# Optimization experiments

Measured on AMD Instinct MI355X. Metric: run time of the kernel, lower is better.

The kernel has to match this reference:

```python
import jax, jax.numpy as jnp
import numpy as np

N_NODES = 50000
N_EDGES = 800000
N_FEAT = 512
N_HID = 256
N_LAYER = 4
N_CLASS = 40


def setup_inputs() -> dict:
    key = jax.random.key(0)
    ks = jax.random.split(key, 16)
    x = jax.random.normal(ks[0], (N_NODES, N_FEAT), dtype=jnp.float32)
    edge_index = jax.random.randint(ks[1], (2, N_EDGES), 0, N_NODES, dtype=jnp.int64 if jax.config.jax_enable_x64 else jnp.int32)

    def glorot(k, fan_in, fan_out):
        lim = np.sqrt(6.0 / (fan_in + fan_out)).astype(np.float32)
        return jax.random.uniform(k, (fan_in, fan_out), jnp.float32, -lim, lim)

    in_gc_W = glorot(ks[2], N_FEAT, N_HID)
    in_gc_b = jnp.zeros((N_HID,), jnp.float32)
    in_lin_W = glorot(ks[3], N_FEAT, N_HID)
    in_lin_b = jnp.zeros((N_HID,), jnp.float32)
    # n_layer-1 = 3 hidden conv / lin pairs, stacked on leading axis
    convs_W = jnp.stack([glorot(jax.random.fold_in(ks[4], i), N_HID, N_HID) for i in range(N_LAYER - 1)])
    convs_b = jnp.zeros((N_LAYER - 1, N_HID), jnp.float32)
    lins_W = jnp.stack([glorot(jax.random.fold_in(ks[5], i), N_HID, N_HID) for i in range(N_LAYER - 1)])
    lins_b = jnp.zeros((N_LAYER - 1, N_HID), jnp.float32)
    out_W = glorot(ks[6], N_HID * N_LAYER, N_CLASS)
    out_b = jnp.zeros((N_CLASS,), jnp.float32)
    return {
        "x": x, "edge_index": edge_index,
        "in_gc_W": in_gc_W, "in_gc_b": in_gc_b,
        "in_lin_W": in_lin_W, "in_lin_b": in_lin_b,
        "convs_W": convs_W, "convs_b": convs_b,
        "lins_W": lins_W, "lins_b": lins_b,
        "out_W": out_W, "out_b": out_b,
    }


def reference(x, edge_index, in_gc_W, in_gc_b, in_lin_W, in_lin_b,
              convs_W, convs_b, lins_W, lins_b, out_W, out_b):
    src, dst = edge_index[0], edge_index[1]
    n = x.shape[0]
    # GCN symmetric normalization with self-loops: deg = 1 + in-degree
    deg = jnp.zeros((n,), jnp.float32).at[dst].add(1.0) + 1.0
    dinv = jax.lax.rsqrt(deg)
    edge_norm = dinv[src] * dinv[dst]        # [E]
    self_norm = dinv * dinv                  # [N]

    def gcn(h, W, b):
        hw = h @ W                           # [N, out]
        msg = hw[src] * edge_norm[:, None]   # gather + scale
        agg = jax.ops.segment_sum(msg, dst, num_segments=n)
        agg = agg + hw * self_norm[:, None]  # self-loop term
        return agg + b

    # inductive: GCNConv + linear residual; dropout = identity (eval mode)
    h = jax.nn.relu(gcn(x, in_gc_W, in_gc_b) + x @ in_lin_W + in_lin_b)
    xs = [h]
    for i in range(convs_W.shape[0]):
        h = jax.nn.relu(gcn(h, convs_W[i], convs_b[i]) + h @ lins_W[i] + lins_b[i])
        xs.append(h)
    # JumpingKnowledge mode='cat'
    jk = jnp.concatenate(xs, axis=-1)        # [N, n_hid * n_layer]
    return jk @ out_W + out_b
```

## Files before the change

### kernel.cpp

```cpp
#include <hip/hip_runtime.h>

typedef _Float16 half8 __attribute__((ext_vector_type(8)));
typedef _Float16 half4 __attribute__((ext_vector_type(4)));
typedef float floatx4 __attribute__((ext_vector_type(4)));

__device__ __forceinline__ void gld16(const _Float16* g, _Float16* lds_base) {
    __builtin_amdgcn_global_load_lds(
        (const __attribute__((address_space(1))) unsigned int*)g,
        (__attribute__((address_space(3))) unsigned int*)lds_base,
        16, 0, 0);
}

__global__ __launch_bounds__(256) void zero_i32(int* __restrict__ p, int n) {
    int i = blockIdx.x * 256 + threadIdx.x;
    if (i < n) p[i] = 0;
}

__global__ __launch_bounds__(256) void hist_dst(const int* __restrict__ dst,
                                                int* __restrict__ count, int E) {
    int e = blockIdx.x * 256 + threadIdx.x;
    if (e < E) atomicAdd(&count[dst[e]], 1);
}

__global__ __launch_bounds__(256) void make_dinv(const int* __restrict__ count,
                                                 float* __restrict__ dinv, int n) {
    int i = blockIdx.x * 256 + threadIdx.x;
    if (i < n) dinv[i] = rsqrtf(1.0f + (float)count[i]);
}

__global__ __launch_bounds__(256) void cast_f32_f16(const float* __restrict__ in,
                                                    _Float16* __restrict__ out, int n4) {
    int i = blockIdx.x * 256 + threadIdx.x;
    if (i < n4) {
        float4 v = *(const float4*)&in[(size_t)i * 4];
        half4 h = { (_Float16)v.x, (_Float16)v.y, (_Float16)v.z, (_Float16)v.w };
        *(half4*)&out[(size_t)i * 4] = h;
    }
}

__global__ __launch_bounds__(256) void transpose_cast(const float* __restrict__ W,
                                                      _Float16* __restrict__ WT,
                                                      int K, int N) {
    int k = blockIdx.x;
    int n = threadIdx.x;
    if (n < N) WT[(size_t)n * K + k] = (_Float16)W[(size_t)k * N + n];
}

__global__ __launch_bounds__(256) void scan_block(const int* __restrict__ count,
                                                  int* __restrict__ incl,
                                                  int* __restrict__ blocksum, int n) {
    __shared__ int tmp[256];
    int t = threadIdx.x;
    int i = blockIdx.x * 256 + t;
    int v = (i < n) ? count[i] : 0;
    tmp[t] = v;
    __syncthreads();
    for (int off = 1; off < 256; off <<= 1) {
        int x = (t >= off) ? tmp[t - off] : 0;
        __syncthreads();
        tmp[t] += x;
        __syncthreads();
    }
    if (i < n) incl[i] = tmp[t];
    if (t == 255) blocksum[blockIdx.x] = tmp[255];
}

__global__ __launch_bounds__(256) void scan_top(const int* __restrict__ blocksum,
                                                int* __restrict__ blockoff, int nb) {
    __shared__ int tmp[256];
    int t = threadIdx.x;
    int v = (t < nb) ? blocksum[t] : 0;
    tmp[t] = v;
    __syncthreads();
    for (int off = 1; off < 256; off <<= 1) {
        int x = (t >= off) ? tmp[t - off] : 0;
        __syncthreads();
        tmp[t] += x;
        __syncthreads();
    }
    if (t < nb) blockoff[t] = tmp[t] - v;
}

__global__ __launch_bounds__(256) void make_rowptr(const int* __restrict__ incl,
                                                   const int* __restrict__ count,
                                                   const int* __restrict__ blockoff,
                                                   int* __restrict__ rowptr,
                                                   int* __restrict__ cursor, int n) {
    int i = blockIdx.x * 256 + threadIdx.x;
    if (i < n) {
        int r = incl[i] - count[i] + blockoff[blockIdx.x];
        rowptr[i] = r;
        cursor[i] = r;
    }
}

__global__ __launch_bounds__(256) void scatter_perm(const int* __restrict__ src,
                                                    const int* __restrict__ dst,
                                                    const float* __restrict__ dinv,
                                                    int* __restrict__ cursor,
                                                    int* __restrict__ sorted_src,
                                                    float* __restrict__ sorted_norm, int E) {
    int e = blockIdx.x * 256 + threadIdx.x;
    if (e < E) {
        int d = dst[e], s = src[e];
        int slot = atomicAdd(&cursor[d], 1);
        sorted_src[slot] = s;
        sorted_norm[slot] = dinv[s] * dinv[d];
    }
}

template<bool DUAL>
__global__ __launch_bounds__(256) void gemm_mfma(
    const _Float16* __restrict__ A, int lda,
    const _Float16* __restrict__ BT, int Nrows,
    const float* __restrict__ bias0, const float* __restrict__ bias1,
    _Float16* __restrict__ lin_h, _Float16* __restrict__ hw,
    float* __restrict__ Cf, int ldc,
    int M, int K)
{
    __shared__ _Float16 As[128 * 64];
    __shared__ _Float16 Bs[128 * 64];

    const int tid  = threadIdx.x;
    const int wave = tid >> 6;
    const int lane = tid & 63;
    const int q    = lane >> 4;
    const int r    = lane & 15;

    const int wm = (wave & 1) * 64;
    const int wn = (wave >> 1) * 64;

    const int bn = blockIdx.x * 128;
    const int bm = blockIdx.y * 128;

    const int srow  = wave * 32;
    const int lrow8 = lane >> 3;
    const int cp    = lane & 7;

    floatx4 acc[4][4] = {};

    for (int k0 = 0; k0 < K; k0 += 64) {
        #pragma unroll
        for (int t = 0; t < 4; ++t) {
            int lrow = srow + t * 8 + lrow8;
            int c    = cp ^ (lrow & 7);
            int gm = bm + lrow; if (gm > M - 1) gm = M - 1;
            gld16(&A[(size_t)gm * lda + k0 + c * 8], &As[(srow + t * 8) * 64]);
            int gn = bn + lrow; if (gn > Nrows - 1) gn = Nrows - 1;
            gld16(&BT[(size_t)gn * K + k0 + c * 8], &Bs[(srow + t * 8) * 64]);
        }
        __syncthreads();

        #pragma unroll
        for (int kk = 0; kk < 2; ++kk) {
            const int sc = ((kk << 2) | q) ^ (r & 7);
            half8 af[4], bf[4];
            #pragma unroll
            for (int mi = 0; mi < 4; ++mi)
                af[mi] = *(const half8*)&As[(wm + mi * 16 + r) * 64 + sc * 8];
            #pragma unroll
            for (int ni = 0; ni < 4; ++ni)
                bf[ni] = *(const half8*)&Bs[(wn + ni * 16 + r) * 64 + sc * 8];
            #pragma unroll
            for (int mi = 0; mi < 4; ++mi)
                #pragma unroll
                for (int ni = 0; ni < 4; ++ni)
                    acc[mi][ni] = __builtin_amdgcn_mfma_f32_16x16x32_f16(
                        af[mi], bf[ni], acc[mi][ni], 0, 0, 0);
        }
        __syncthreads();
    }

    if (DUAL) {
        const bool islin = (bn < 256);
        _Float16* dstp = islin ? lin_h : hw;
        #pragma unroll
        for (int ni = 0; ni < 4; ++ni) {
            int col = bn + wn + ni * 16 + r;
            int c2  = islin ? col : col - 256;
            float badd = islin ? (bias0[col] + bias1[col]) : 0.0f;
            #pragma unroll
            for (int mi = 0; mi < 4; ++mi)
                #pragma unroll
                for (int reg = 0; reg < 4; ++reg) {
                    int gm = bm + wm + mi * 16 + q * 4 + reg;
                    if (gm < M)
                        dstp[(size_t)gm * 256 + c2] = (_Float16)(acc[mi][ni][reg] + badd);
                }
        }
    } else {
        #pragma unroll
        for (int ni = 0; ni < 4; ++ni) {
            int col = bn + wn + ni * 16 + r;
            if (col >= Nrows) continue;
            float badd = bias0 ? bias0[col] : 0.0f;
            #pragma unroll
            for (int mi = 0; mi < 4; ++mi)
                #pragma unroll
                for (int reg = 0; reg < 4; ++reg) {
                    int gm = bm + wm + mi * 16 + q * 4 + reg;
                    if (gm < M)
                        Cf[(size_t)gm * ldc + col] = acc[mi][ni][reg] + badd;
                }
        }
    }
}

__global__ __launch_bounds__(256) void aggregate_csr(
    const int* __restrict__ rowptr, const int* __restrict__ count,
    const int* __restrict__ sorted_src, const float* __restrict__ sorted_norm,
    const float* __restrict__ dinv,
    const _Float16* __restrict__ hw,
    const _Float16* __restrict__ lin_h,
    _Float16* __restrict__ jk_col, int n)
{
    int wave = (blockIdx.x * 256 + threadIdx.x) >> 6;
    int lane = threadIdx.x & 63;
    if (wave >= n) return;
    const int i = wave;

    const int start = rowptr[i];
    const int deg   = count[i];

    half4 l4 = *(const half4*)&lin_h[(size_t)i * 256 + lane * 4];
    float4 acc = make_float4((float)l4[0], (float)l4[1], (float)l4[2], (float)l4[3]);

    for (int base = 0; base < deg; base += 64) {
        int m = deg - base;
        if (m > 64) m = 64;
        int   s_l  = 0;
        float nm_l = 0.0f;
        if (lane < m) {
            s_l  = sorted_src[start + base + lane];
            nm_l = sorted_norm[start + base + lane];
        }
        for (int j = 0; j < m; j += 4) {
            half4 hv[4];
            float nm[4];
            #pragma unroll
            for (int k2 = 0; k2 < 4; ++k2) {
                int jj  = j + k2;
                int idx = (jj < m) ? jj : (m - 1);
                int s   = __shfl(s_l, idx, 64);
                nm[k2]  = (jj < m) ? __shfl(nm_l, jj, 64) : 0.0f;
                hv[k2]  = *(const half4*)&hw[(size_t)s * 256 + lane * 4];
            }
            #pragma unroll
            for (int k2 = 0; k2 < 4; ++k2) {
                acc.x = fmaf((float)hv[k2][0], nm[k2], acc.x);
                acc.y = fmaf((float)hv[k2][1], nm[k2], acc.y);
                acc.z = fmaf((float)hv[k2][2], nm[k2], acc.z);
                acc.w = fmaf((float)hv[k2][3], nm[k2], acc.w);
            }
        }
    }

    float di = dinv[i];
    float sn = di * di;
    half4 hs = *(const half4*)&hw[(size_t)i * 256 + lane * 4];
    acc.x = fmaxf(fmaf((float)hs[0], sn, acc.x), 0.0f);
    acc.y = fmaxf(fmaf((float)hs[1], sn, acc.y), 0.0f);
    acc.z = fmaxf(fmaf((float)hs[2], sn, acc.z), 0.0f);
    acc.w = fmaxf(fmaf((float)hs[3], sn, acc.w), 0.0f);

    half4 o = { (_Float16)acc.x, (_Float16)acc.y, (_Float16)acc.z, (_Float16)acc.w };
    *(half4*)&jk_col[(size_t)i * 1024 + lane * 4] = o;
}

extern "C" void kernel_launch(void* const* d_in, const int* in_sizes, int n_in,
                              void* d_out, int out_size, void* d_ws, size_t ws_size,
                              hipStream_t stream) {
    const float* x        = (const float*)d_in[0];
    const int*   ei       = (const int*)d_in[1];
    const float* in_gc_W  = (const float*)d_in[2];
    const float* in_gc_b  = (const float*)d_in[3];
    const float* in_lin_W = (const float*)d_in[4];
    const float* in_lin_b = (const float*)d_in[5];
    const float* convs_W  = (const float*)d_in[6];
    const float* convs_b  = (const float*)d_in[7];
    const float* lins_W   = (const float*)d_in[8];
    const float* lins_b   = (const float*)d_in[9];
    const float* out_W    = (const float*)d_in[10];
    const float* out_b    = (const float*)d_in[11];

    const int N = 50000;
    const int E = in_sizes[1] / 2;
    const int F = 512, H = 256, L = 4, NC = 40;

    const int* src = ei;
    const int* dst = ei + E;

    char* ws = (char*)d_ws;
    auto carve = [&](size_t bytes) { void* p = ws; ws += (bytes + 255) & ~(size_t)255; return p; };
    float*    dinv       = (float*)carve((size_t)N * 4);
    int*      count      = (int*)  carve((size_t)N * 4);
    int*      incl       = (int*)  carve((size_t)N * 4);
    int*      rowptr     = (int*)  carve((size_t)N * 4);
    int*      cursor     = (int*)  carve((size_t)N * 4);
    int*      blocksum   = (int*)  carve(256 * 4);
    int*      blockoff   = (int*)  carve(256 * 4);
    int*      sorted_src = (int*)  carve((size_t)E * 4);
    float*    sorted_nrm = (float*)carve((size_t)E * 4);
    _Float16* xh         = (_Float16*)carve((size_t)N * F * 2);
    _Float16* w0comb     = (_Float16*)carve((size_t)512 * F * 2);
    _Float16* wcomb      = (_Float16*)carve((size_t)3 * 512 * H * 2);
    _Float16* outWT      = (_Float16*)carve((size_t)NC * H * L * 2);
    _Float16* lin_h      = (_Float16*)carve((size_t)N * H * 2);
    _Float16* hw         = (_Float16*)carve((size_t)N * H * 2);
    _Float16* jk_h       = (_Float16*)carve((size_t)N * H * L * 2);
    float*    out        = (float*)d_out;

    const int nbN = (N + 255) / 256;
    const int nbE = (E + 255) / 256;

    zero_i32<<<nbN, 256, 0, stream>>>(count, N);
    hist_dst<<<nbE, 256, 0, stream>>>(dst, count, E);
    make_dinv<<<nbN, 256, 0, stream>>>(count, dinv, N);
    scan_block<<<nbN, 256, 0, stream>>>(count, incl, blocksum, N);
    scan_top<<<1, 256, 0, stream>>>(blocksum, blockoff, nbN);
    make_rowptr<<<nbN, 256, 0, stream>>>(incl, count, blockoff, rowptr, cursor, N);
    scatter_perm<<<nbE, 256, 0, stream>>>(src, dst, dinv, cursor, sorted_src, sorted_nrm, E);

    cast_f32_f16<<<(N * F / 4 + 255) / 256, 256, 0, stream>>>(x, xh, N * F / 4);
    transpose_cast<<<F, 256, 0, stream>>>(in_lin_W, w0comb,               F, H);
    transpose_cast<<<F, 256, 0, stream>>>(in_gc_W,  w0comb + (size_t)H * F, F, H);
    for (int l = 0; l < 3; ++l) {
        _Float16* wl = wcomb + (size_t)l * 512 * H;
        transpose_cast<<<H, 256, 0, stream>>>(lins_W  + (size_t)l * H * H, wl,                   H, H);
        transpose_cast<<<H, 256, 0, stream>>>(convs_W + (size_t)l * H * H, wl + (size_t)H * H,   H, H);
    }
    transpose_cast<<<H * L, 256, 0, stream>>>(out_W, outWT, H * L, NC);

    const dim3 dgrid(4, (N + 127) / 128);
    const dim3 ogrid(1, (N + 127) / 128);
    const int agg_blocks = (N + 3) / 4;

    for (int l = 0; l < L; ++l) {
        const _Float16* Ah = (l == 0) ? xh : (jk_h + (size_t)(l - 1) * H);
        int lda            = (l == 0) ? F : H * L;
        int K              = (l == 0) ? F : H;
        const _Float16* BT = (l == 0) ? w0comb : (wcomb + (size_t)(l - 1) * 512 * H);
        const float* gcB   = (l == 0) ? in_gc_b  : (convs_b + (size_t)(l - 1) * H);
        const float* liB   = (l == 0) ? in_lin_b : (lins_b  + (size_t)(l - 1) * H);

        gemm_mfma<true><<<dgrid, 256, 0, stream>>>(Ah, lda, BT, 512, liB, gcB,
                                                   lin_h, hw, nullptr, 0, N, K);
        aggregate_csr<<<agg_blocks, 256, 0, stream>>>(rowptr, count, sorted_src, sorted_nrm,
                                                      dinv, hw, lin_h, jk_h + (size_t)l * H, N);
    }

    gemm_mfma<false><<<ogrid, 256, 0, stream>>>(jk_h, H * L, outWT, NC, out_b, nullptr,
                                                nullptr, nullptr, out, NC, N, H * L);
}
```

Before: 746.5 us.

## Pack CSR metadata, widen aggregation loads, fuse dinv, tile weight transposes

Stores each edge's source index and normalisation together as an int2, so aggregation does one load and two shuffles per edge instead of two separate arrays. The aggregation kernel now splits each wave into two half-waves that each read 16-byte half8 rows for alternating edges, then combines the halves with an xor-shuffle. That doubles the edges in flight per iteration but performs a cross-lane reduction and leaves half the lanes idle at the store. Separately, dinv is computed inside scan_block, removing one launch, and the weight transposes use a 32x32 LDS-tiled kernel for coalesced writes.

```diff
diff --git a/kernel.cpp b/kernel.cpp
--- a/kernel.cpp
+++ b/kernel.cpp
@@ -20,12 +20,6 @@
                                                 int* __restrict__ count, int E) {
     int e = blockIdx.x * 256 + threadIdx.x;
     if (e < E) atomicAdd(&count[dst[e]], 1);
-}
-
-__global__ __launch_bounds__(256) void make_dinv(const int* __restrict__ count,
-                                                 float* __restrict__ dinv, int n) {
-    int i = blockIdx.x * 256 + threadIdx.x;
-    if (i < n) dinv[i] = rsqrtf(1.0f + (float)count[i]);
 }
 
 __global__ __launch_bounds__(256) void cast_f32_f16(const float* __restrict__ in,
@@ -38,21 +32,35 @@
     }
 }
 
-__global__ __launch_bounds__(256) void transpose_cast(const float* __restrict__ W,
-                                                      _Float16* __restrict__ WT,
-                                                      int K, int N) {
-    int k = blockIdx.x;
-    int n = threadIdx.x;
-    if (n < N) WT[(size_t)n * K + k] = (_Float16)W[(size_t)k * N + n];
+__global__ __launch_bounds__(256) void transpose_cast_tiled(
+    const float* __restrict__ W, _Float16* __restrict__ WT, int K, int N)
+{
+    __shared__ _Float16 t[32][33];
+    const int k0 = blockIdx.x * 32, n0 = blockIdx.y * 32;
+    const int tx = threadIdx.x & 31, ty = threadIdx.x >> 5;
+    #pragma unroll
+    for (int i = 0; i < 4; ++i) {
+        int k = k0 + ty + i * 8, n = n0 + tx;
+        float v = (k < K && n < N) ? W[(size_t)k * N + n] : 0.0f;
+        t[ty + i * 8][tx] = (_Float16)v;
+    }
+    __syncthreads();
+    #pragma unroll
+    for (int i = 0; i < 4; ++i) {
+        int n = n0 + ty + i * 8, k = k0 + tx;
+        if (n < N && k < K) WT[(size_t)n * K + k] = t[tx][ty + i * 8];
+    }
 }
 
 __global__ __launch_bounds__(256) void scan_block(const int* __restrict__ count,
                                                   int* __restrict__ incl,
-                                                  int* __restrict__ blocksum, int n) {
+                                                  int* __restrict__ blocksum,
+                                                  float* __restrict__ dinv, int n) {
     __shared__ int tmp[256];
     int t = threadIdx.x;
     int i = blockIdx.x * 256 + t;
     int v = (i < n) ? count[i] : 0;
+    if (i < n) dinv[i] = rsqrtf(1.0f + (float)v);
     tmp[t] = v;
     __syncthreads();
     for (int off = 1; off < 256; off <<= 1) {
@@ -98,14 +106,12 @@
                                                     const int* __restrict__ dst,
                                                     const float* __restrict__ dinv,
                                                     int* __restrict__ cursor,
-                                                    int* __restrict__ sorted_src,
-                                                    float* __restrict__ sorted_norm, int E) {
+                                                    int2* __restrict__ sorted_meta, int E) {
     int e = blockIdx.x * 256 + threadIdx.x;
     if (e < E) {
         int d = dst[e], s = src[e];
         int slot = atomicAdd(&cursor[d], 1);
-        sorted_src[slot] = s;
-        sorted_norm[slot] = dinv[s] * dinv[d];
+        sorted_meta[slot] = make_int2(s, __float_as_int(dinv[s] * dinv[d]));
     }
 }
 
@@ -208,7 +214,7 @@
 
 __global__ __launch_bounds__(256) void aggregate_csr(
     const int* __restrict__ rowptr, const int* __restrict__ count,
-    const int* __restrict__ sorted_src, const float* __restrict__ sorted_norm,
+    const int2* __restrict__ sorted_meta,
     const float* __restrict__ dinv,
     const _Float16* __restrict__ hw,
     const _Float16* __restrict__ lin_h,
@@ -218,53 +224,61 @@
     int lane = threadIdx.x & 63;
     if (wave >= n) return;
     const int i = wave;
+    const int h  = lane >> 5;
+    const int fl = lane & 31;
 
     const int start = rowptr[i];
     const int deg   = count[i];
 
-    half4 l4 = *(const half4*)&lin_h[(size_t)i * 256 + lane * 4];
-    float4 acc = make_float4((float)l4[0], (float)l4[1], (float)l4[2], (float)l4[3]);
+    float accf[8];
+    if (h == 0) {
+        half8 l8 = *(const half8*)&lin_h[(size_t)i * 256 + fl * 8];
+        #pragma unroll
+        for (int t = 0; t < 8; ++t) accf[t] = (float)l8[t];
+    } else {
+        float di = dinv[i];
+        float sn = di * di;
+        half8 s8 = *(const half8*)&hw[(size_t)i * 256 + fl * 8];
+        #pragma unroll
+        for (int t = 0; t < 8; ++t) accf[t] = (float)s8[t] * sn;
+    }
 
     for (int base = 0; base < deg; base += 64) {
         int m = deg - base;
         if (m > 64) m = 64;
-        int   s_l  = 0;
-        float nm_l = 0.0f;
-        if (lane < m) {
-            s_l  = sorted_src[start + base + lane];
-            nm_l = sorted_norm[start + base + lane];
-        }
-        for (int j = 0; j < m; j += 4) {
-            half4 hv[4];
+        int2 meta = make_int2(0, 0);
+        if (lane < m) meta = sorted_meta[start + base + lane];
+
+        for (int j = 0; j < m; j += 8) {
+            half8 hv[4];
             float nm[4];
             #pragma unroll
             for (int k2 = 0; k2 < 4; ++k2) {
-                int jj  = j + k2;
-                int idx = (jj < m) ? jj : (m - 1);
-                int s   = __shfl(s_l, idx, 64);
-                nm[k2]  = (jj < m) ? __shfl(nm_l, jj, 64) : 0.0f;
-                hv[k2]  = *(const half4*)&hw[(size_t)s * 256 + lane * 4];
+                int e   = j + k2 * 2 + h;
+                int idx = (e < m) ? e : (m - 1);
+                int s   = __shfl(meta.x, idx, 64);
+                int nmb = __shfl(meta.y, idx, 64);
+                nm[k2]  = (e < m) ? __int_as_float(nmb) : 0.0f;
+                hv[k2]  = *(const half8*)&hw[(size_t)s * 256 + fl * 8];
             }
             #pragma unroll
-            for (int k2 = 0; k2 < 4; ++k2) {
-                acc.x = fmaf((float)hv[k2][0], nm[k2], acc.x);
-                acc.y = fmaf((float)hv[k2][1], nm[k2], acc.y);
-                acc.z = fmaf((float)hv[k2][2], nm[k2], acc.z);
-                acc.w = fmaf((float)hv[k2][3], nm[k2], acc.w);
-            }
-        }
-    }
-
-    float di = dinv[i];
-    float sn = di * di;
-    half4 hs = *(const half4*)&hw[(size_t)i * 256 + lane * 4];
-    acc.x = fmaxf(fmaf((float)hs[0], sn, acc.x), 0.0f);
-    acc.y = fmaxf(fmaf((float)hs[1], sn, acc.y), 0.0f);
-    acc.z = fmaxf(fmaf((float)hs[2], sn, acc.z), 0.0f);
-    acc.w = fmaxf(fmaf((float)hs[3], sn, acc.w), 0.0f);
-
-    half4 o = { (_Float16)acc.x, (_Float16)acc.y, (_Float16)acc.z, (_Float16)acc.w };
-    *(half4*)&jk_col[(size_t)i * 1024 + lane * 4] = o;
+            for (int k2 = 0; k2 < 4; ++k2)
+                #pragma unroll
+                for (int t = 0; t < 8; ++t)
+                    accf[t] = fmaf((float)hv[k2][t], nm[k2], accf[t]);
+        }
+    }
+
+    #pragma unroll
+    for (int t = 0; t < 8; ++t)
+        accf[t] += __shfl_xor(accf[t], 32, 64);
+
+    if (h == 0) {
+        half8 o;
+        #pragma unroll
+        for (int t = 0; t < 8; ++t) o[t] = (_Float16)fmaxf(accf[t], 0.0f);
+        *(half8*)&jk_col[(size_t)i * 1024 + fl * 8] = o;
+    }
 }
 
 extern "C" void kernel_launch(void* const* d_in, const int* in_sizes, int n_in,
@@ -292,44 +306,47 @@
 
     char* ws = (char*)d_ws;
     auto carve = [&](size_t bytes) { void* p = ws; ws += (bytes + 255) & ~(size_t)255; return p; };
-    float*    dinv       = (float*)carve((size_t)N * 4);
-    int*      count      = (int*)  carve((size_t)N * 4);
-    int*      incl       = (int*)  carve((size_t)N * 4);
-    int*      rowptr     = (int*)  carve((size_t)N * 4);
-    int*      cursor     = (int*)  carve((size_t)N * 4);
-    int*      blocksum   = (int*)  carve(256 * 4);
-    int*      blockoff   = (int*)  carve(256 * 4);
-    int*      sorted_src = (int*)  carve((size_t)E * 4);
-    float*    sorted_nrm = (float*)carve((size_t)E * 4);
-    _Float16* xh         = (_Float16*)carve((size_t)N * F * 2);
-    _Float16* w0comb     = (_Float16*)carve((size_t)512 * F * 2);
-    _Float16* wcomb      = (_Float16*)carve((size_t)3 * 512 * H * 2);
-    _Float16* outWT      = (_Float16*)carve((size_t)NC * H * L * 2);
-    _Float16* lin_h      = (_Float16*)carve((size_t)N * H * 2);
-    _Float16* hw         = (_Float16*)carve((size_t)N * H * 2);
-    _Float16* jk_h       = (_Float16*)carve((size_t)N * H * L * 2);
-    float*    out        = (float*)d_out;
+    float*    dinv        = (float*)carve((size_t)N * 4);
+    int*      count       = (int*)  carve((size_t)N * 4);
+    int*      incl        = (int*)  carve((size_t)N * 4);
+    int*      rowptr      = (int*)  carve((size_t)N * 4);
+    int*      cursor      = (int*)  carve((size_t)N * 4);
+    int*      blocksum    = (int*)  carve(256 * 4);
+    int*      blockoff    = (int*)  carve(256 * 4);
+    int2*     sorted_meta = (int2*) carve((size_t)E * 8);
+    _Float16* xh          = (_Float16*)carve((size_t)N * F * 2);
+    _Float16* w0comb      = (_Float16*)carve((size_t)512 * F * 2);
+    _Float16* wcomb       = (_Float16*)carve((size_t)3 * 512 * H * 2);
+    _Float16* outWT       = (_Float16*)carve((size_t)NC * H * L * 2);
+    _Float16* lin_h       = (_Float16*)carve((size_t)N * H * 2);
+    _Float16* hw          = (_Float16*)carve((size_t)N * H * 2);
+    _Float16* jk_h        = (_Float16*)carve((size_t)N * H * L * 2);
+    float*    out         = (float*)d_out;
 
     const int nbN = (N + 255) / 256;
     const int nbE = (E + 255) / 256;
 
     zero_i32<<<nbN, 256, 0, stream>>>(count, N);
     hist_dst<<<nbE, 256, 0, stream>>>(dst, count, E);
-    make_dinv<<<nbN, 256, 0, stream>>>(count, dinv, N);
-    scan_block<<<nbN, 256, 0, stream>>>(count, incl, blocksum, N);
+    scan_block<<<nbN, 256, 0, stream>>>(count, incl, blocksum, dinv, N);
     scan_top<<<1, 256, 0, stream>>>(blocksum, blockoff, nbN);
     make_rowptr<<<nbN, 256, 0, stream>>>(incl, count, blockoff, rowptr, cursor, N);
-    scatter_perm<<<nbE, 256, 0, stream>>>(src, dst, dinv, cursor, sorted_src, sorted_nrm, E);
+    scatter_perm<<<nbE, 256, 0, stream>>>(src, dst, dinv, cursor, sorted_meta, E);
 
     cast_f32_f16<<<(N * F / 4 + 255) / 256, 256, 0, stream>>>(x, xh, N * F / 4);
-    transpose_cast<<<F, 256, 0, stream>>>(in_lin_W, w0comb,               F, H);
-    transpose_cast<<<F, 256, 0, stream>>>(in_gc_W,  w0comb + (size_t)H * F, F, H);
-    for (int l = 0; l < 3; ++l) {
-        _Float16* wl = wcomb + (size_t)l * 512 * H;
-        transpose_cast<<<H, 256, 0, stream>>>(lins_W  + (size_t)l * H * H, wl,                   H, H);
-        transpose_cast<<<H, 256, 0, stream>>>(convs_W + (size_t)l * H * H, wl + (size_t)H * H,   H, H);
-    }
-    transpose_cast<<<H * L, 256, 0, stream>>>(out_W, outWT, H * L, NC);
+    {
+        dim3 tg((F + 31) / 32, (H + 31) / 32);
+        transpose_cast_tiled<<<tg, 256, 0, stream>>>(in_lin_W, w0comb,                F, H);
+        transpose_cast_tiled<<<tg, 256, 0, stream>>>(in_gc_W,  w0comb + (size_t)H * F, F, H);
+        dim3 th((H + 31) / 32, (H + 31) / 32);
+        for (int l = 0; l < 3; ++l) {
+            _Float16* wl = wcomb + (size_t)l * 512 * H;
+            transpose_cast_tiled<<<th, 256, 0, stream>>>(lins_W  + (size_t)l * H * H, wl,                 H, H);
+            transpose_cast_tiled<<<th, 256, 0, stream>>>(convs_W + (size_t)l * H * H, wl + (size_t)H * H, H, H);
+        }
+        dim3 to((H * L + 31) / 32, (NC + 31) / 32);
+        transpose_cast_tiled<<<to, 256, 0, stream>>>(out_W, outWT, H * L, NC);
+    }
 
     const dim3 dgrid(4, (N + 127) / 128);
     const dim3 ogrid(1, (N + 127) / 128);
@@ -345,7 +362,7 @@
 
         gemm_mfma<true><<<dgrid, 256, 0, stream>>>(Ah, lda, BT, 512, liB, gcB,
                                                    lin_h, hw, nullptr, 0, N, K);
-        aggregate_csr<<<agg_blocks, 256, 0, stream>>>(rowptr, count, sorted_src, sorted_nrm,
+        aggregate_csr<<<agg_blocks, 256, 0, stream>>>(rowptr, count, sorted_meta,
                                                       dinv, hw, lin_h, jk_h + (size_t)l * H, N);
     }
 
```

Result: no change. 740.9 us (-0.7%).
